# Kernel tuning notes

Hardware: AMD Instinct MI355X
Metric: run time of the kernel (lower is better)

## Reference

```python
import jax, jax.numpy as jnp
import numpy as np

M, U, H, C, EMB, HID = 4096, 8, 8, 64, 64, 128
N = M * U            # 32768 nodes
E = 131072           # edges
D = H * C            # 512 = heads * hidden_channels
NUM_LAYERS = 4
IN0 = 6              # 2 coords + mask + speed + cost + arrival
SCALE = np.float32(1.0 / np.sqrt(C))

def _lin(x, W, b):
    return x @ W + b

def _transformer_conv(x, src, dst, Wq, bq, Wk, bk, Wv, bv, Ws, bs):
    # PyG TransformerConv: x_j = x[src], x_i = x[dst]; softmax over edges per dst
    n = x.shape[0]
    q = _lin(x, Wq, bq).reshape(n, H, C)
    k = _lin(x, Wk, bk).reshape(n, H, C)
    v = _lin(x, Wv, bv).reshape(n, H, C)
    alpha = jnp.einsum('ehc,ehc->eh', q[dst], k[src]) * SCALE   # [E,H]
    amax = jax.ops.segment_max(alpha, dst, num_segments=n)       # [N,H]
    ex = jnp.exp(alpha - amax[dst])
    denom = jax.ops.segment_sum(ex, dst, num_segments=n)         # [N,H]
    agg = jax.ops.segment_sum(ex[:, :, None] * v[src], dst, num_segments=n)  # [N,H,C]
    out = agg / (denom[:, :, None] + 1e-16)
    return out.reshape(n, D) + _lin(x, Ws, bs)                   # concat heads + root skip

def _forward(mission_coords, uavs_info, speeds, cost_matrix, arrival_times,
             Wq0, bq0, Wk0, bk0, Wv0, bv0, Ws0, bs0,
             Wq, bq, Wk, bk, Wv, bv, Ws, bs,
             fc_W, fc_b, aW1, ab1, aW2, ab2, cW1, cb1, cW2, cb2,
             edge_index, batch, action_mask):
    mc = jnp.broadcast_to(mission_coords[:, None, :], (M, U, 2))
    mk = jnp.broadcast_to(action_mask[:, None, None].astype(jnp.float32), (M, U, 1))
    sp = jnp.broadcast_to(speeds[None, :, None], (M, U, 1))
    cm = cost_matrix.T[:, :, None]
    at = arrival_times.T[:, :, None]
    x = jnp.concatenate([mc, mk, sp, cm, at], axis=-1).reshape(N, IN0)
    src, dst = edge_index[0], edge_index[1]
    x = jax.nn.relu(_transformer_conv(x, src, dst, Wq0, bq0, Wk0, bk0, Wv0, bv0, Ws0, bs0))
    for l in range(NUM_LAYERS - 1):
        x = jax.nn.relu(_transformer_conv(x, src, dst, Wq[l], bq[l], Wk[l], bk[l], Wv[l], bv[l], Ws[l], bs[l]))
    new_batch = jnp.repeat(batch, U)                             # [N]
    sums = jax.ops.segment_sum(x, new_batch, num_segments=1)
    cnts = jax.ops.segment_sum(jnp.ones((N,), x.dtype), new_batch, num_segments=1)
    pooled = sums / cnts[:, None]                                # [1, D]
    emb = _lin(pooled, fc_W, fc_b)                               # [1, EMB]
    emb_exp = jnp.tile(emb, (U, 1))                              # [U, EMB]
    combined = jnp.concatenate([uavs_info, emb_exp, speeds[:, None]], axis=-1)  # [U, EMB+3]
    action_probs = jax.nn.softmax(_lin(jax.nn.relu(_lin(combined, aW1, ab1)), aW2, ab2), axis=-1)
    state_values = _lin(jax.nn.relu(_lin(combined, cW1, cb1)), cW2, cb2)
    return action_probs, state_values

def setup_inputs() -> dict:
    key = jax.random.key(0)
    ks = jax.random.split(key, 40)
    def nrm(i, shape, s=0.05):
        return jax.random.normal(ks[i], shape, jnp.float32) * s
    z = lambda *s: jnp.zeros(s, jnp.float32)
    L = NUM_LAYERS - 1
    inp = dict(
        mission_coords=jax.random.uniform(ks[0], (M, 2), jnp.float32),
        uavs_info=nrm(1, (U, 2), 1.0),
        speeds=jax.random.uniform(ks[2], (U,), jnp.float32) + 0.5,
        cost_matrix=jax.random.uniform(ks[3], (U, M), jnp.float32),
        arrival_times=jax.random.uniform(ks[4], (U, M), jnp.float32),
        edge_index=jax.random.randint(ks[5], (2, E), 0, N),
        batch=jnp.zeros((M,), jnp.int32),
        action_mask=jax.random.randint(ks[6], (M,), 0, 2),
        Wq0=nrm(7, (IN0, D)), bq0=z(D), Wk0=nrm(8, (IN0, D)), bk0=z(D),
        Wv0=nrm(9, (IN0, D)), bv0=z(D), Ws0=nrm(10, (IN0, D)), bs0=z(D),
        Wq=nrm(11, (L, D, D)), bq=z(L, D), Wk=nrm(12, (L, D, D)), bk=z(L, D),
        Wv=nrm(13, (L, D, D)), bv=z(L, D), Ws=nrm(14, (L, D, D)), bs=z(L, D),
        fc_W=nrm(15, (D, EMB)), fc_b=z(EMB),
        aW1=nrm(16, (EMB + 3, HID)), ab1=z(HID), aW2=nrm(17, (HID, M)), ab2=z(M),
        cW1=nrm(18, (EMB + 3, HID)), cb1=z(HID), cW2=nrm(19, (HID, 1)), cb2=z(1),
    )
    return inp

def reference(mission_coords, edge_index, batch, uavs_info, action_mask, speeds,
              cost_matrix, arrival_times,
              Wq0, bq0, Wk0, bk0, Wv0, bv0, Ws0, bs0,
              Wq, bq, Wk, bk, Wv, bv, Ws, bs,
              fc_W, fc_b, aW1, ab1, aW2, ab2, cW1, cb1, cW2, cb2):
    return _forward(mission_coords, uavs_info, speeds, cost_matrix, arrival_times,
                    Wq0, bq0, Wk0, bk0, Wv0, bv0, Ws0, bs0,
                    Wq, bq, Wk, bk, Wv, bv, Ws, bs,
                    fc_W, fc_b, aW1, ab1, aW2, ab2, cW1, cb1, cW2, cb2,
                    edge_index, batch, action_mask)
```

## Files before the change

### kernel.cpp

```cpp
#include <hip/hip_runtime.h>
#include <stdint.h>

typedef unsigned char u8;
typedef unsigned short u16;
typedef unsigned long long u64;
typedef __attribute__((ext_vector_type(8))) unsigned short u16x8;
typedef __attribute__((ext_vector_type(8))) __bf16 bf16x8;
typedef __attribute__((ext_vector_type(4))) float f32x4;
typedef __attribute__((ext_vector_type(2))) float f32x2;

#define NNODES 32768
#define NEDGES 131072
#define DDIM 512
#define QK4 2048
#define MM 4096
#define UU 8


__device__ __forceinline__ u16 f2bf(float f) {
    unsigned u = __builtin_bit_cast(unsigned, f);
    u += 0x7FFFu + ((u >> 16) & 1u);
    return (u16)(u >> 16);
}
__device__ __forceinline__ float bf2f(u16 h) {
    return __builtin_bit_cast(float, (unsigned)h << 16);
}
__device__ __forceinline__ void enc8(const float* f, int* lo, int* hi) {
    int a = __builtin_amdgcn_cvt_pk_fp8_f32(f[0], f[1], 0, false);
    a = __builtin_amdgcn_cvt_pk_fp8_f32(f[2], f[3], a, true);
    int b = __builtin_amdgcn_cvt_pk_fp8_f32(f[4], f[5], 0, false);
    b = __builtin_amdgcn_cvt_pk_fp8_f32(f[6], f[7], b, true);
    *lo = a;
    *hi = b;
}
__device__ __forceinline__ void dec8(int lo, int hi, float* f) {
    f32x2 a = __builtin_amdgcn_cvt_pk_f32_fp8(lo, false);
    f32x2 b = __builtin_amdgcn_cvt_pk_f32_fp8(lo, true);
    f32x2 c = __builtin_amdgcn_cvt_pk_f32_fp8(hi, false);
    f32x2 d = __builtin_amdgcn_cvt_pk_f32_fp8(hi, true);
    f[0] = a[0]; f[1] = a[1]; f[2] = b[0]; f[3] = b[1];
    f[4] = c[0]; f[5] = c[1]; f[6] = d[0]; f[7] = d[1];
}

__device__ __forceinline__ void load_lds16(const void* g, void* l) {
    __builtin_amdgcn_global_load_lds((__attribute__((address_space(1))) unsigned int*)(void*)g,
                                     (__attribute__((address_space(3))) unsigned int*)l, 16, 0, 0);
}

__global__ void k_prep(const float* __restrict__ mc, const int* __restrict__ mask,
                       const float* __restrict__ sp, const float* __restrict__ cm,
                       const float* __restrict__ at, float* __restrict__ x0,
                       const float* __restrict__ Wq0, const float* __restrict__ Wk0,
                       const float* __restrict__ Wv0, const float* __restrict__ Ws0,
                       float* __restrict__ W0cat,
                       const float* __restrict__ bq0, const float* __restrict__ bk0,
                       const float* __restrict__ bv0, const float* __restrict__ bs0,
                       const float* __restrict__ bq, const float* __restrict__ bk,
                       const float* __restrict__ bv, const float* __restrict__ bs,
                       float* __restrict__ b0cat, float* __restrict__ bcat,
                       int* __restrict__ deg, float* __restrict__ pooled) {
    int b = blockIdx.x;
    int t = threadIdx.x;
    if (b < 128) {
        int node = b * 256 + t;
        deg[node] = 0;
        int m = node >> 3, u = node & 7;
        float* o = x0 + (size_t)node * 6;
        o[0] = mc[m * 2];
        o[1] = mc[m * 2 + 1];
        o[2] = (float)mask[m];
        o[3] = sp[u];
        o[4] = cm[u * MM + m];
        o[5] = at[u * MM + m];
    } else if (b < 176) {
        int i = (b - 128) * 256 + t;
        int k = i / QK4, n = i % QK4;
        int ty = n >> 9, nn = n & 511;
        const float* p = (ty == 0) ? Wq0 : (ty == 1) ? Wk0 : (ty == 2) ? Wv0 : Ws0;
        W0cat[i] = p[k * DDIM + nn];
    } else if (b < 208) {
        int i = (b - 176) * 256 + t;
        int n = i & (QK4 - 1);
        int l = i >> 11;
        int ty = n >> 9, nn = n & 511;
        if (l == 0) {
            const float* p = (ty == 0) ? bq0 : (ty == 1) ? bk0 : (ty == 2) ? bv0 : bs0;
            b0cat[n] = p[nn];
        } else {
            const float* p = (ty == 0) ? bq : (ty == 1) ? bk : (ty == 2) ? bv : bs;
            bcat[(size_t)(l - 1) * QK4 + n] = p[(l - 1) * DDIM + nn];
        }
    } else {
        pooled[(b - 208) * 256 + t] = 0.f;
    }
}

__global__ void k_wt(const float* __restrict__ Wq, const float* __restrict__ Wk,
                     const float* __restrict__ Wv, const float* __restrict__ Ws,
                     u16* __restrict__ Wt) {
    __shared__ float tile[32][33];
    int q = blockIdx.z;
    int l = q >> 2, t = q & 3;
    const float* src = ((t == 0) ? Wq : (t == 1) ? Wk : (t == 2) ? Wv : Ws) + (size_t)l * DDIM * DDIM;
    int k0 = blockIdx.x * 32, n0 = blockIdx.y * 32;
    int tx = threadIdx.x, ty = threadIdx.y;
#pragma unroll
    for (int r = 0; r < 4; r++) tile[ty + 8 * r][tx] = src[(size_t)(k0 + ty + 8 * r) * DDIM + n0 + tx];
    __syncthreads();
    u16* dst = Wt + (size_t)l * QK4 * DDIM + (size_t)t * DDIM * DDIM;
#pragma unroll
    for (int r = 0; r < 4; r++) {
        int n = n0 + ty + 8 * r;
        dst[(size_t)n * DDIM + k0 + tx] = f2bf(tile[tx][ty + 8 * r]);
    }
}

__global__ void k_count(const int* __restrict__ dst, int* __restrict__ deg) {
    int e = blockIdx.x * 256 + threadIdx.x;
    if (e < NEDGES) atomicAdd(&deg[dst[e]], 1);
}

__global__ __launch_bounds__(1024) void k_scan(const int* __restrict__ deg, int* __restrict__ offs,
                                               int* __restrict__ cursor) {
    __shared__ int sums[1024];
    int t = threadIdx.x;
    int base = t * 32;
    int local[32];
    int s = 0;
#pragma unroll
    for (int i = 0; i < 32; i++) { local[i] = s; s += deg[base + i]; }
    sums[t] = s;
    __syncthreads();
    for (int d = 1; d < 1024; d <<= 1) {
        int v = (t >= d) ? sums[t - d] : 0;
        __syncthreads();
        sums[t] += v;
        __syncthreads();
    }
    int excl = (t == 0) ? 0 : sums[t - 1];
#pragma unroll
    for (int i = 0; i < 32; i++) {
        int o = excl + local[i];
        offs[base + i] = o;
        cursor[base + i] = o;
    }
    if (t == 1023) offs[NNODES] = sums[1023];
}

__global__ void k_scatter(const int* __restrict__ src, const int* __restrict__ dst,
                          int* __restrict__ cursor, int* __restrict__ ssrc) {
    int e = blockIdx.x * 256 + threadIdx.x;
    if (e < NEDGES) {
        int pos = atomicAdd(&cursor[dst[e]], 1);
        ssrc[pos] = src[e];
    }
}

__global__ __launch_bounds__(256) void k_gemm0(const float* __restrict__ x0, const float* __restrict__ W0cat,
                                               const float* __restrict__ b0cat, u8* __restrict__ Q8,
                                               u8* __restrict__ KV8, u16* __restrict__ S16) {
    int node = blockIdx.x;
    int t = threadIdx.x;
    float xv[6];
#pragma unroll
    for (int k = 0; k < 6; k++) xv[k] = x0[(size_t)node * 6 + k];
    int n0 = t * 8;
    float f[8];
#pragma unroll
    for (int j = 0; j < 8; j++) {
        int n = n0 + j;
        float s = b0cat[n];
#pragma unroll
        for (int k = 0; k < 6; k++) s += xv[k] * W0cat[k * QK4 + n];
        f[j] = s;
    }
    if (n0 < 512) {
        int lo, hi;
        enc8(f, &lo, &hi);
        *(int2*)(Q8 + (size_t)node * 512 + n0) = make_int2(lo, hi);
    } else if (n0 < 1536) {
        int lo, hi;
        enc8(f, &lo, &hi);
        int kvcol = (n0 < 1024) ? (n0 - 512) : (n0 - 1024);
        int ofs = (n0 < 1024) ? 0 : 8;
        *(int2*)(KV8 + (size_t)node * 1024 + (size_t)(kvcol >> 3) * 16 + ofs) = make_int2(lo, hi);
    } else {
        u16x8 o;
#pragma unroll
        for (int j = 0; j < 8; j++) o[j] = f2bf(f[j]);
        *(u16x8*)(S16 + (size_t)node * 512 + (n0 - 1536)) = o;
    }
}

__global__ __launch_bounds__(256, 4) void k_gemm(const u16* __restrict__ X, const u16* __restrict__ Wt,
                                                 const float* __restrict__ bcat, u8* __restrict__ Q8,
                                                 u8* __restrict__ KV8, u16* __restrict__ S16) {
    __shared__ __align__(16) u16 smem[2 * 128 * 64];
    u16* As = smem;
    u16* Bs = smem + 128 * 64;
    const int tid = threadIdx.x;
    const int lane = tid & 63;
    const int w = tid >> 6;
    const int wm = w & 1, wn = w >> 1;
    const int bid = blockIdx.x;
    const int xcd = bid & 7;
    const int s = bid >> 3;
    const size_t arow0 = (size_t)(xcd * 32 + (s >> 4)) * 128;
    const size_t brow0 = (size_t)(s & 15) * 128;
    const int bt = (int)(brow0 >> 7);

    f32x4 acc[4][4];
#pragma unroll
    for (int i = 0; i < 4; i++)
#pragma unroll
        for (int j = 0; j < 4; j++) acc[i][j] = (f32x4){0.f, 0.f, 0.f, 0.f};

    const int la = lane & 7;
    const int quad = lane >> 4;
    const int lm = lane & 15;

    for (int kt = 0; kt < 8; ++kt) {
        const int k0 = kt * 64;
#pragma unroll
        for (int t = 0; t < 4; ++t) {
            int idx = (w * 4 + t) * 64 + lane;
            int m = idx >> 3;
            int c = la ^ (m & 7);
            const u16* ga = X + (arow0 + m) * DDIM + (k0 + c * 8);
            const u16* gb = Wt + (brow0 + m) * DDIM + (k0 + c * 8);
            load_lds16(ga, &As[(size_t)((w * 4 + t) * 64) * 8]);
            load_lds16(gb, &Bs[(size_t)((w * 4 + t) * 64) * 8]);
        }
        __syncthreads();
#pragma unroll
        for (int kk = 0; kk < 2; ++kk) {
            bf16x8 af[4], bfg[4];
            int c = kk * 4 + quad;
#pragma unroll
            for (int i = 0; i < 4; ++i) {
                int m = wm * 64 + i * 16 + lm;
                int slot = m * 8 + (c ^ (m & 7));
                af[i] = *(const bf16x8*)&As[(size_t)slot * 8];
            }
#pragma unroll
            for (int j = 0; j < 4; ++j) {
                int n = wn * 64 + j * 16 + lm;
                int slot = n * 8 + (c ^ (n & 7));
                bfg[j] = *(const bf16x8*)&Bs[(size_t)slot * 8];
            }
#pragma unroll
            for (int i = 0; i < 4; ++i)
#pragma unroll
                for (int j = 0; j < 4; ++j)
                    acc[i][j] = __builtin_amdgcn_mfma_f32_16x16x32_bf16(af[i], bfg[j], acc[i][j], 0, 0, 0);
        }
        __syncthreads();
    }

    float biasv[4];
#pragma unroll
    for (int j = 0; j < 4; ++j) biasv[j] = bcat[brow0 + wn * 64 + j * 16 + lm];

    u16* stg = smem;
    const int chunk = lane & 7;
    const int rrow = lane >> 3;
    const int colbase = (int)brow0 + wn * 64 + chunk * 8;
#pragma unroll
    for (int p = 0; p < 2; ++p) {
        __syncthreads();
#pragma unroll
        for (int ii = 0; ii < 2; ++ii) {
            int i = p * 2 + ii;
#pragma unroll
            for (int j = 0; j < 4; ++j) {
#pragma unroll
                for (int r = 0; r < 4; ++r) {
                    int lr = ii * 16 + quad * 4 + r;
                    int lc = j * 16 + lm;
                    stg[(size_t)(w * 32 + lr) * 72 + lc] = f2bf(acc[i][j][r] + biasv[j]);
                }
            }
        }
        __syncthreads();
#pragma unroll
        for (int it = 0; it < 4; ++it) {
            int row = it * 8 + rrow;
            u16x8 v = *(const u16x8*)&stg[(size_t)(w * 32 + row) * 72 + chunk * 8];
            size_t grow = arow0 + wm * 64 + p * 32 + row;
            if (bt < 4) {
                float f[8];
#pragma unroll
                for (int j = 0; j < 8; j++) f[j] = bf2f(v[j]);
                int lo, hi;
                enc8(f, &lo, &hi);
                *(int2*)(Q8 + grow * 512 + colbase) = make_int2(lo, hi);
            } else if (bt < 12) {
                float f[8];
#pragma unroll
                for (int j = 0; j < 8; j++) f[j] = bf2f(v[j]);
                int lo, hi;
                enc8(f, &lo, &hi);
                int kvcol = (bt < 8) ? (colbase - 512) : (colbase - 1024);
                int ofs = (bt < 8) ? 0 : 8;
                *(int2*)(KV8 + grow * 1024 + (size_t)(kvcol >> 3) * 16 + ofs) = make_int2(lo, hi);
            } else {
                *(u16x8*)(S16 + grow * 512 + (colbase - 1536)) = v;
            }
        }
    }
}

__global__ __launch_bounds__(256) void k_attn(const u8* __restrict__ Q8, const u8* __restrict__ KV8,
                                              const u16* __restrict__ S16, const int* __restrict__ offs,
                                              const int* __restrict__ ssrc, u16* __restrict__ Xout) {
    const int lane = threadIdx.x & 63;
    const int node = blockIdx.x * 4 + (threadIdx.x >> 6);
    const u64 q8 = *(const u64*)(Q8 + (size_t)node * 512 + (size_t)lane * 8);
    float qf[8];
    dec8((int)(q8 & 0xFFFFFFFFull), (int)(q8 >> 32), qf);
    float m = -INFINITY, l = 0.f;
    float acc[8];
#pragma unroll
    for (int j = 0; j < 8; j++) acc[j] = 0.f;
    const int e0 = offs[node], e1 = offs[node + 1];
    int4 kvn;
    if (e0 < e1) kvn = *(const int4*)(KV8 + (size_t)ssrc[e0] * 1024 + (size_t)lane * 16);
    for (int e = e0; e < e1; ++e) {
        int4 kv = kvn;
        if (e + 1 < e1) kvn = *(const int4*)(KV8 + (size_t)ssrc[e + 1] * 1024 + (size_t)lane * 16);
        f32x2 k01 = __builtin_amdgcn_cvt_pk_f32_fp8(kv.x, false);
        f32x2 k23 = __builtin_amdgcn_cvt_pk_f32_fp8(kv.x, true);
        f32x2 k45 = __builtin_amdgcn_cvt_pk_f32_fp8(kv.y, false);
        f32x2 k67 = __builtin_amdgcn_cvt_pk_f32_fp8(kv.y, true);
        float d = qf[0] * k01[0] + qf[1] * k01[1] + qf[2] * k23[0] + qf[3] * k23[1] +
                  qf[4] * k45[0] + qf[5] * k45[1] + qf[6] * k67[0] + qf[7] * k67[1];
        d += __shfl_xor(d, 1, 64);
        d += __shfl_xor(d, 2, 64);
        d += __shfl_xor(d, 4, 64);
        float a = d * 0.125f;
        float nm = fmaxf(m, a);
        float corr = __expf(m - nm);
        float p = __expf(a - nm);
        l = l * corr + p;
        f32x2 v01 = __builtin_amdgcn_cvt_pk_f32_fp8(kv.z, false);
        f32x2 v23 = __builtin_amdgcn_cvt_pk_f32_fp8(kv.z, true);
        f32x2 v45 = __builtin_amdgcn_cvt_pk_f32_fp8(kv.w, false);
        f32x2 v67 = __builtin_amdgcn_cvt_pk_f32_fp8(kv.w, true);
        acc[0] = acc[0] * corr + p * v01[0];
        acc[1] = acc[1] * corr + p * v01[1];
        acc[2] = acc[2] * corr + p * v23[0];
        acc[3] = acc[3] * corr + p * v23[1];
        acc[4] = acc[4] * corr + p * v45[0];
        acc[5] = acc[5] * corr + p * v45[1];
        acc[6] = acc[6] * corr + p * v67[0];
        acc[7] = acc[7] * corr + p * v67[1];
        m = nm;
    }
    float inv = 1.0f / (l + 1e-16f);
    const u16x8 sv = *(const u16x8*)(S16 + (size_t)node * 512 + (size_t)lane * 8);
    u16x8 o;
#pragma unroll
    for (int j = 0; j < 8; j++) {
        float r = acc[j] * inv + bf2f(sv[j]);
        o[j] = f2bf(fmaxf(r, 0.f));
    }
    *(u16x8*)(Xout + (size_t)node * DDIM + (size_t)lane * 8) = o;
}

__global__ __launch_bounds__(256) void k_pool(const u16* __restrict__ X, float* __restrict__ pooled) {
    __shared__ float red[4][64][8];
    int t = threadIdx.x;
    int chunk = t & 63;
    int rofs = t >> 6;
    float s[8];
#pragma unroll
    for (int j = 0; j < 8; j++) s[j] = 0.f;
    int nd0 = blockIdx.x * 256;
    for (int nd = nd0 + rofs; nd < nd0 + 256; nd += 4) {
        u16x8 v = *(const u16x8*)&X[(size_t)nd * DDIM + chunk * 8];
#pragma unroll
        for (int j = 0; j < 8; j++) s[j] += bf2f(v[j]);
    }
#pragma unroll
    for (int j = 0; j < 8; j++) red[rofs][chunk][j] = s[j];
    __syncthreads();
    if (t < 64) {
#pragma unroll
        for (int j = 0; j < 8; j++) {
            float o = red[0][t][j] + red[1][t][j] + red[2][t][j] + red[3][t][j];
            atomicAdd(&pooled[t * 8 + j], o);
        }
    }
}

__global__ __launch_bounds__(1024) void k_heads(const float* __restrict__ pooled, const float* __restrict__ fcW,
                                                const float* __restrict__ fcb, const float* __restrict__ ui,
                                                const float* __restrict__ sp, const float* __restrict__ aW1,
                                                const float* __restrict__ ab1, const float* __restrict__ cW1,
                                                const float* __restrict__ cb1, const float* __restrict__ cW2,
                                                const float* __restrict__ cb2, float* __restrict__ hidden_a,
                                                float* __restrict__ out) {
    __shared__ float spool[512];
    __shared__ float semb[64];
    __shared__ float shc[8][128];
    int t = threadIdx.x;
    if (t < 512) spool[t] = pooled[t] * (1.0f / 32768.0f);
    __syncthreads();
    if (t < 64) {
        float s = fcb[t];
        for (int k = 0; k < 512; k++) s += spool[k] * fcW[k * 64 + t];
        semb[t] = s;
    }
    __syncthreads();
    int u = t >> 7, j = t & 127;
    float u0 = ui[u * 2], u1 = ui[u * 2 + 1], uspd = sp[u];
    float ha = ab1[j] + u0 * aW1[j] + u1 * aW1[128 + j] + uspd * aW1[66 * 128 + j];
    float hc = cb1[j] + u0 * cW1[j] + u1 * cW1[128 + j] + uspd * cW1[66 * 128 + j];
    for (int k = 0; k < 64; k++) {
        float e = semb[k];
        ha += e * aW1[(2 + k) * 128 + j];
        hc += e * cW1[(2 + k) * 128 + j];
    }
    ha = fmaxf(ha, 0.f);
    hc = fmaxf(hc, 0.f);
    hidden_a[u * 128 + j] = ha;
    shc[u][j] = hc;
    __syncthreads();
    if (t < 8) {
        float s = cb2[0];
        for (int k = 0; k < 128; k++) s += shc[t][k] * cW2[k];
        out[NNODES + t] = s;
    }
}

__global__ __launch_bounds__(1024) void k_actor(const float* __restrict__ hidden_a, const float* __restrict__ aW2,
                                                const float* __restrict__ ab2, float* __restrict__ out) {
    __shared__ float h[128];
    __shared__ float red[1024];
    int u = blockIdx.x, t = threadIdx.x;
    if (t < 128) h[t] = hidden_a[u * 128 + t];
    __syncthreads();
    float lg[4];
#pragma unroll
    for (int p = 0; p < 4; p++) {
        int mcol = t + p * 1024;
        float s = ab2[mcol];
        for (int k = 0; k < 128; k++) s += h[k] * aW2[(size_t)k * MM + mcol];
        lg[p] = s;
    }
    float mx = fmaxf(fmaxf(lg[0], lg[1]), fmaxf(lg[2], lg[3]));
    red[t] = mx;
    __syncthreads();
    for (int s2 = 512; s2 > 0; s2 >>= 1) {
        if (t < s2) red[t] = fmaxf(red[t], red[t + s2]);
        __syncthreads();
    }
    mx = red[0];
    __syncthreads();
    float e[4], sum = 0.f;
#pragma unroll
    for (int p = 0; p < 4; p++) {
        e[p] = __expf(lg[p] - mx);
        sum += e[p];
    }
    red[t] = sum;
    __syncthreads();
    for (int s2 = 512; s2 > 0; s2 >>= 1) {
        if (t < s2) red[t] += red[t + s2];
        __syncthreads();
    }
    float inv = 1.0f / red[0];
#pragma unroll
    for (int p = 0; p < 4; p++) out[(size_t)u * MM + t + p * 1024] = e[p] * inv;
}

extern "C" void kernel_launch(void* const* d_in, const int* in_sizes, int n_in,
                              void* d_out, int out_size, void* d_ws, size_t ws_size,
                              hipStream_t stream) {
    const float* mc   = (const float*)d_in[0];
    const float* ui   = (const float*)d_in[1];
    const float* sp   = (const float*)d_in[2];
    const float* cm   = (const float*)d_in[3];
    const float* at   = (const float*)d_in[4];
    const int*   eidx = (const int*)d_in[5];
    const int*   mask = (const int*)d_in[7];
    const float* Wq0 = (const float*)d_in[8];
    const float* bq0 = (const float*)d_in[9];
    const float* Wk0 = (const float*)d_in[10];
    const float* bk0 = (const float*)d_in[11];
    const float* Wv0 = (const float*)d_in[12];
    const float* bv0 = (const float*)d_in[13];
    const float* Ws0 = (const float*)d_in[14];
    const float* bs0 = (const float*)d_in[15];
    const float* Wq = (const float*)d_in[16];
    const float* bq = (const float*)d_in[17];
    const float* Wk = (const float*)d_in[18];
    const float* bk = (const float*)d_in[19];
    const float* Wv = (const float*)d_in[20];
    const float* bv = (const float*)d_in[21];
    const float* Ws = (const float*)d_in[22];
    const float* bs = (const float*)d_in[23];
    const float* fcW = (const float*)d_in[24];
    const float* fcb = (const float*)d_in[25];
    const float* aW1 = (const float*)d_in[26];
    const float* ab1 = (const float*)d_in[27];
    const float* aW2 = (const float*)d_in[28];
    const float* ab2 = (const float*)d_in[29];
    const float* cW1 = (const float*)d_in[30];
    const float* cb1 = (const float*)d_in[31];
    const float* cW2 = (const float*)d_in[32];
    const float* cb2 = (const float*)d_in[33];
    float* out = (float*)d_out;

    const int* esrc = eidx;
    const int* edst = eidx + NEDGES;

    char* ws = (char*)d_ws;
    size_t off = 0;
    auto alloc = [&](size_t bytes) -> void* {
        void* p = ws + off;
        off += (bytes + 255) & ~(size_t)255;
        return p;
    };
    u8*    Q8    = (u8*)alloc((size_t)NNODES * 512);
    u8*    KV8   = (u8*)alloc((size_t)NNODES * 1024);
    u16*   S16   = (u16*)alloc((size_t)NNODES * 512 * 2);
    u16*   X     = (u16*)alloc((size_t)NNODES * DDIM * 2);
    u16*   Wt    = (u16*)alloc((size_t)3 * QK4 * DDIM * 2);
    float* W0cat = (float*)alloc((size_t)6 * QK4 * 4);
    float* b0cat = (float*)alloc((size_t)QK4 * 4);
    float* bcat  = (float*)alloc((size_t)3 * QK4 * 4);
    float* x0    = (float*)alloc((size_t)NNODES * 6 * 4);
    int*   deg   = (int*)alloc((size_t)NNODES * 4);
    int*   offs  = (int*)alloc((size_t)(NNODES + 1) * 4);
    int*   cursor= (int*)alloc((size_t)NNODES * 4);
    int*   ssrc  = (int*)alloc((size_t)NEDGES * 4);
    float* pooled= (float*)alloc((size_t)512 * 4);
    float* hidden_a = (float*)alloc((size_t)UU * 128 * 4);
    (void)ws_size; (void)in_sizes; (void)n_in; (void)out_size;

    k_prep<<<210, 256, 0, stream>>>(mc, mask, sp, cm, at, x0, Wq0, Wk0, Wv0, Ws0, W0cat,
                                    bq0, bk0, bv0, bs0, bq, bk, bv, bs, b0cat, bcat, deg, pooled);
    {
        dim3 g(16, 16, 12), b(32, 8);
        k_wt<<<g, b, 0, stream>>>(Wq, Wk, Wv, Ws, Wt);
    }
    k_count<<<NEDGES / 256, 256, 0, stream>>>(edst, deg);
    k_scan<<<1, 1024, 0, stream>>>(deg, offs, cursor);
    k_scatter<<<NEDGES / 256, 256, 0, stream>>>(esrc, edst, cursor, ssrc);

    k_gemm0<<<NNODES, 256, 0, stream>>>(x0, W0cat, b0cat, Q8, KV8, S16);
    k_attn<<<NNODES / 4, 256, 0, stream>>>(Q8, KV8, S16, offs, ssrc, X);

    for (int l = 0; l < 3; ++l) {
        k_gemm<<<4096, 256, 0, stream>>>(X, Wt + (size_t)l * QK4 * DDIM, bcat + (size_t)l * QK4, Q8, KV8, S16);
        k_attn<<<NNODES / 4, 256, 0, stream>>>(Q8, KV8, S16, offs, ssrc, X);
    }

    k_pool<<<128, 256, 0, stream>>>(X, pooled);
    k_heads<<<1, 1024, 0, stream>>>(pooled, fcW, fcb, ui, sp, aW1, ab1, cW1, cb1, cW2, cb2, hidden_a, out);
    k_actor<<<UU, 1024, 0, stream>>>(hidden_a, aW2, ab2, out);
}
```

Before: 631.0 us.

## Collapse first TransformerConv layer into low-rank bilinear attention on 6-dim inputs

Layer 0 inputs have only 6 features, so the per-head score q_i·k_j is rewritten as a 6x6 bilinear form plus linear and constant terms, precomputed once in a tiny kernel. The attention loop then aggregates the raw 6-dim source features weighted by softmax, and projects them through Wv0 afterwards, which removes the layer-0 gemm and its Q/KV/S writes and reads. Separately, the main attention loop now loads up to four neighbour KV rows at once instead of prefetching one ahead. This adds more per-edge scalar arithmetic and larger register pressure in k_attn0, and skips the fp8 quantisation the old layer-0 path applied to Q, K and V.

```diff
diff --git a/kernel.cpp b/kernel.cpp
--- a/kernel.cpp
+++ b/kernel.cpp
@@ -50,14 +50,9 @@
 __global__ void k_prep(const float* __restrict__ mc, const int* __restrict__ mask,
                        const float* __restrict__ sp, const float* __restrict__ cm,
                        const float* __restrict__ at, float* __restrict__ x0,
-                       const float* __restrict__ Wq0, const float* __restrict__ Wk0,
-                       const float* __restrict__ Wv0, const float* __restrict__ Ws0,
-                       float* __restrict__ W0cat,
-                       const float* __restrict__ bq0, const float* __restrict__ bk0,
-                       const float* __restrict__ bv0, const float* __restrict__ bs0,
                        const float* __restrict__ bq, const float* __restrict__ bk,
                        const float* __restrict__ bv, const float* __restrict__ bs,
-                       float* __restrict__ b0cat, float* __restrict__ bcat,
+                       float* __restrict__ bcat,
                        int* __restrict__ deg, float* __restrict__ pooled) {
     int b = blockIdx.x;
     int t = threadIdx.x;
@@ -72,27 +67,39 @@
         o[3] = sp[u];
         o[4] = cm[u * MM + m];
         o[5] = at[u * MM + m];
-    } else if (b < 176) {
+    } else if (b < 152) {
         int i = (b - 128) * 256 + t;
-        int k = i / QK4, n = i % QK4;
-        int ty = n >> 9, nn = n & 511;
-        const float* p = (ty == 0) ? Wq0 : (ty == 1) ? Wk0 : (ty == 2) ? Wv0 : Ws0;
-        W0cat[i] = p[k * DDIM + nn];
-    } else if (b < 208) {
-        int i = (b - 176) * 256 + t;
         int n = i & (QK4 - 1);
         int l = i >> 11;
         int ty = n >> 9, nn = n & 511;
-        if (l == 0) {
-            const float* p = (ty == 0) ? bq0 : (ty == 1) ? bk0 : (ty == 2) ? bv0 : bs0;
-            b0cat[n] = p[nn];
-        } else {
-            const float* p = (ty == 0) ? bq : (ty == 1) ? bk : (ty == 2) ? bv : bs;
-            bcat[(size_t)(l - 1) * QK4 + n] = p[(l - 1) * DDIM + nn];
-        }
+        const float* p = (ty == 0) ? bq : (ty == 1) ? bk : (ty == 2) ? bv : bs;
+        bcat[(size_t)l * QK4 + n] = p[l * DDIM + nn];
     } else {
-        pooled[(b - 208) * 256 + t] = 0.f;
-    }
+        pooled[(b - 152) * 256 + t] = 0.f;
+    }
+}
+
+__global__ void k_c0(const float* __restrict__ Wq0, const float* __restrict__ bq0,
+                     const float* __restrict__ Wk0, const float* __restrict__ bk0,
+                     float* __restrict__ C0) {
+    int i = threadIdx.x;
+    if (i >= 392) return;
+    int h = i / 49, r = i % 49;
+    int d0 = h * 64;
+    float s = 0.f;
+    if (r < 36) {
+        int a = r / 6, b = r % 6;
+        for (int d = 0; d < 64; d++) s += Wq0[a * DDIM + d0 + d] * Wk0[b * DDIM + d0 + d];
+    } else if (r < 42) {
+        int a = r - 36;
+        for (int d = 0; d < 64; d++) s += Wq0[a * DDIM + d0 + d] * bk0[d0 + d];
+    } else if (r < 48) {
+        int b = r - 42;
+        for (int d = 0; d < 64; d++) s += Wk0[b * DDIM + d0 + d] * bq0[d0 + d];
+    } else {
+        for (int d = 0; d < 64; d++) s += bq0[d0 + d] * bk0[d0 + d];
+    }
+    C0[i] = s;
 }
 
 __global__ void k_wt(const float* __restrict__ Wq, const float* __restrict__ Wk,
@@ -156,39 +163,82 @@
     }
 }
 
-__global__ __launch_bounds__(256) void k_gemm0(const float* __restrict__ x0, const float* __restrict__ W0cat,
-                                               const float* __restrict__ b0cat, u8* __restrict__ Q8,
-                                               u8* __restrict__ KV8, u16* __restrict__ S16) {
-    int node = blockIdx.x;
-    int t = threadIdx.x;
-    float xv[6];
-#pragma unroll
-    for (int k = 0; k < 6; k++) xv[k] = x0[(size_t)node * 6 + k];
-    int n0 = t * 8;
-    float f[8];
-#pragma unroll
-    for (int j = 0; j < 8; j++) {
-        int n = n0 + j;
-        float s = b0cat[n];
-#pragma unroll
-        for (int k = 0; k < 6; k++) s += xv[k] * W0cat[k * QK4 + n];
-        f[j] = s;
-    }
-    if (n0 < 512) {
-        int lo, hi;
-        enc8(f, &lo, &hi);
-        *(int2*)(Q8 + (size_t)node * 512 + n0) = make_int2(lo, hi);
-    } else if (n0 < 1536) {
-        int lo, hi;
-        enc8(f, &lo, &hi);
-        int kvcol = (n0 < 1024) ? (n0 - 512) : (n0 - 1024);
-        int ofs = (n0 < 1024) ? 0 : 8;
-        *(int2*)(KV8 + (size_t)node * 1024 + (size_t)(kvcol >> 3) * 16 + ofs) = make_int2(lo, hi);
-    } else {
-        u16x8 o;
-#pragma unroll
-        for (int j = 0; j < 8; j++) o[j] = f2bf(f[j]);
-        *(u16x8*)(S16 + (size_t)node * 512 + (n0 - 1536)) = o;
+__global__ __launch_bounds__(256) void k_attn0(const float* __restrict__ x0, const float* __restrict__ C0,
+                                               const float* __restrict__ Wv0, const float* __restrict__ bv0,
+                                               const float* __restrict__ Ws0, const float* __restrict__ bs0,
+                                               const int* __restrict__ offs, const int* __restrict__ ssrc,
+                                               u16* __restrict__ Xout) {
+    const int lane = threadIdx.x & 63;
+    const int wv = threadIdx.x >> 6;
+    const int h = lane & 7;
+    float wV[8][6], wS[8][6], bV[8], bS[8];
+#pragma unroll
+    for (int j = 0; j < 8; ++j) {
+        int c = lane + 64 * j;
+        bV[j] = bv0[c];
+        bS[j] = bs0[c];
+#pragma unroll
+        for (int a = 0; a < 6; ++a) {
+            wV[j][a] = Wv0[a * DDIM + c];
+            wS[j][a] = Ws0[a * DDIM + c];
+        }
+    }
+    float Ah[36], uh[6], wh[6], ch;
+#pragma unroll
+    for (int r = 0; r < 36; ++r) Ah[r] = C0[h * 49 + r];
+#pragma unroll
+    for (int a = 0; a < 6; ++a) uh[a] = C0[h * 49 + 36 + a];
+#pragma unroll
+    for (int a = 0; a < 6; ++a) wh[a] = C0[h * 49 + 42 + a];
+    ch = C0[h * 49 + 48];
+
+    int node0 = (blockIdx.x * 4 + wv) * 8;
+    for (int nn = 0; nn < 8; ++nn) {
+        int node = node0 + nn;
+        float xi[6];
+#pragma unroll
+        for (int a = 0; a < 6; ++a) xi[a] = x0[(size_t)node * 6 + a];
+        float m = -INFINITY, l = 0.f;
+        float xh[6];
+#pragma unroll
+        for (int a = 0; a < 6; ++a) xh[a] = 0.f;
+        const int e0 = offs[node], e1 = offs[node + 1];
+        for (int e = e0; e < e1; ++e) {
+            int s = ssrc[e];
+            float xj[6];
+#pragma unroll
+            for (int a = 0; a < 6; ++a) xj[a] = x0[(size_t)s * 6 + a];
+            float alpha = ch;
+#pragma unroll
+            for (int a = 0; a < 6; ++a) {
+                float t = uh[a];
+#pragma unroll
+                for (int b = 0; b < 6; ++b) t += Ah[a * 6 + b] * xj[b];
+                alpha += xi[a] * t;
+            }
+#pragma unroll
+            for (int b = 0; b < 6; ++b) alpha += wh[b] * xj[b];
+            alpha *= 0.125f;
+            float nm = fmaxf(m, alpha);
+            float corr = __expf(m - nm);
+            float p = __expf(alpha - nm);
+            l = l * corr + p;
+#pragma unroll
+            for (int a = 0; a < 6; ++a) xh[a] = xh[a] * corr + p * xj[a];
+            m = nm;
+        }
+#pragma unroll
+        for (int j = 0; j < 8; ++j) {
+            float lb = __shfl(l, j, 64);
+            float num = lb * bV[j];
+#pragma unroll
+            for (int a = 0; a < 6; ++a) num += __shfl(xh[a], j, 64) * wV[j][a];
+            float skip = bS[j];
+#pragma unroll
+            for (int a = 0; a < 6; ++a) skip += xi[a] * wS[j][a];
+            float r = num / (lb + 1e-16f) + skip;
+            Xout[(size_t)node * DDIM + lane + 64 * j] = f2bf(fmaxf(r, 0.f));
+        }
     }
 }
 
@@ -323,38 +373,51 @@
 #pragma unroll
     for (int j = 0; j < 8; j++) acc[j] = 0.f;
     const int e0 = offs[node], e1 = offs[node + 1];
-    int4 kvn;
-    if (e0 < e1) kvn = *(const int4*)(KV8 + (size_t)ssrc[e0] * 1024 + (size_t)lane * 16);
-    for (int e = e0; e < e1; ++e) {
-        int4 kv = kvn;
-        if (e + 1 < e1) kvn = *(const int4*)(KV8 + (size_t)ssrc[e + 1] * 1024 + (size_t)lane * 16);
-        f32x2 k01 = __builtin_amdgcn_cvt_pk_f32_fp8(kv.x, false);
-        f32x2 k23 = __builtin_amdgcn_cvt_pk_f32_fp8(kv.x, true);
-        f32x2 k45 = __builtin_amdgcn_cvt_pk_f32_fp8(kv.y, false);
-        f32x2 k67 = __builtin_amdgcn_cvt_pk_f32_fp8(kv.y, true);
-        float d = qf[0] * k01[0] + qf[1] * k01[1] + qf[2] * k23[0] + qf[3] * k23[1] +
-                  qf[4] * k45[0] + qf[5] * k45[1] + qf[6] * k67[0] + qf[7] * k67[1];
-        d += __shfl_xor(d, 1, 64);
-        d += __shfl_xor(d, 2, 64);
-        d += __shfl_xor(d, 4, 64);
-        float a = d * 0.125f;
-        float nm = fmaxf(m, a);
-        float corr = __expf(m - nm);
-        float p = __expf(a - nm);
-        l = l * corr + p;
-        f32x2 v01 = __builtin_amdgcn_cvt_pk_f32_fp8(kv.z, false);
-        f32x2 v23 = __builtin_amdgcn_cvt_pk_f32_fp8(kv.z, true);
-        f32x2 v45 = __builtin_amdgcn_cvt_pk_f32_fp8(kv.w, false);
-        f32x2 v67 = __builtin_amdgcn_cvt_pk_f32_fp8(kv.w, true);
-        acc[0] = acc[0] * corr + p * v01[0];
-        acc[1] = acc[1] * corr + p * v01[1];
-        acc[2] = acc[2] * corr + p * v23[0];
-        acc[3] = acc[3] * corr + p * v23[1];
-        acc[4] = acc[4] * corr + p * v45[0];
-        acc[5] = acc[5] * corr + p * v45[1];
-        acc[6] = acc[6] * corr + p * v67[0];
-        acc[7] = acc[7] * corr + p * v67[1];
-        m = nm;
+    int e = e0;
+    while (e < e1) {
+        int nb = e1 - e;
+        if (nb > 4) nb = 4;
+        int4 kvb[4];
+#pragma unroll
+        for (int i = 0; i < 4; ++i) {
+            if (i < nb) {
+                int s = ssrc[e + i];
+                kvb[i] = *(const int4*)(KV8 + (size_t)s * 1024 + (size_t)lane * 16);
+            }
+        }
+#pragma unroll
+        for (int i = 0; i < 4; ++i) {
+            if (i >= nb) break;
+            int4 kv = kvb[i];
+            f32x2 k01 = __builtin_amdgcn_cvt_pk_f32_fp8(kv.x, false);
+            f32x2 k23 = __builtin_amdgcn_cvt_pk_f32_fp8(kv.x, true);
+            f32x2 k45 = __builtin_amdgcn_cvt_pk_f32_fp8(kv.y, false);
+            f32x2 k67 = __builtin_amdgcn_cvt_pk_f32_fp8(kv.y, true);
+            float d = qf[0] * k01[0] + qf[1] * k01[1] + qf[2] * k23[0] + qf[3] * k23[1] +
+                      qf[4] * k45[0] + qf[5] * k45[1] + qf[6] * k67[0] + qf[7] * k67[1];
+            d += __shfl_xor(d, 1, 64);
+            d += __shfl_xor(d, 2, 64);
+            d += __shfl_xor(d, 4, 64);
+            float a = d * 0.125f;
+            float nm = fmaxf(m, a);
+            float corr = __expf(m - nm);
+            float p = __expf(a - nm);
+            l = l * corr + p;
+            f32x2 v01 = __builtin_amdgcn_cvt_pk_f32_fp8(kv.z, false);
+            f32x2 v23 = __builtin_amdgcn_cvt_pk_f32_fp8(kv.z, true);
+            f32x2 v45 = __builtin_amdgcn_cvt_pk_f32_fp8(kv.w, false);
+            f32x2 v67 = __builtin_amdgcn_cvt_pk_f32_fp8(kv.w, true);
+            acc[0] = acc[0] * corr + p * v01[0];
+            acc[1] = acc[1] * corr + p * v01[1];
+            acc[2] = acc[2] * corr + p * v23[0];
+            acc[3] = acc[3] * corr + p * v23[1];
+            acc[4] = acc[4] * corr + p * v45[0];
+            acc[5] = acc[5] * corr + p * v45[1];
+            acc[6] = acc[6] * corr + p * v67[0];
+            acc[7] = acc[7] * corr + p * v67[1];
+            m = nm;
+        }
+        e += nb;
     }
     float inv = 1.0f / (l + 1e-16f);
     const u16x8 sv = *(const u16x8*)(S16 + (size_t)node * 512 + (size_t)lane * 8);
@@ -527,9 +590,8 @@
     u16*   S16   = (u16*)alloc((size_t)NNODES * 512 * 2);
     u16*   X     = (u16*)alloc((size_t)NNODES * DDIM * 2);
     u16*   Wt    = (u16*)alloc((size_t)3 * QK4 * DDIM * 2);
-    float* W0cat = (float*)alloc((size_t)6 * QK4 * 4);
-    float* b0cat = (float*)alloc((size_t)QK4 * 4);
     float* bcat  = (float*)alloc((size_t)3 * QK4 * 4);
+    float* C0    = (float*)alloc((size_t)392 * 4);
     float* x0    = (float*)alloc((size_t)NNODES * 6 * 4);
     int*   deg   = (int*)alloc((size_t)NNODES * 4);
     int*   offs  = (int*)alloc((size_t)(NNODES + 1) * 4);
@@ -539,8 +601,8 @@
     float* hidden_a = (float*)alloc((size_t)UU * 128 * 4);
     (void)ws_size; (void)in_sizes; (void)n_in; (void)out_size;
 
-    k_prep<<<210, 256, 0, stream>>>(mc, mask, sp, cm, at, x0, Wq0, Wk0, Wv0, Ws0, W0cat,
-                                    bq0, bk0, bv0, bs0, bq, bk, bv, bs, b0cat, bcat, deg, pooled);
+    k_prep<<<154, 256, 0, stream>>>(mc, mask, sp, cm, at, x0, bq, bk, bv, bs, bcat, deg, pooled);
+    k_c0<<<1, 512, 0, stream>>>(Wq0, bq0, Wk0, bk0, C0);
     {
         dim3 g(16, 16, 12), b(32, 8);
         k_wt<<<g, b, 0, stream>>>(Wq, Wk, Wv, Ws, Wt);
@@ -549,8 +611,7 @@
     k_scan<<<1, 1024, 0, stream>>>(deg, offs, cursor);
     k_scatter<<<NEDGES / 256, 256, 0, stream>>>(esrc, edst, cursor, ssrc);
 
-    k_gemm0<<<NNODES, 256, 0, stream>>>(x0, W0cat, b0cat, Q8, KV8, S16);
-    k_attn<<<NNODES / 4, 256, 0, stream>>>(Q8, KV8, S16, offs, ssrc, X);
+    k_attn0<<<1024, 256, 0, stream>>>(x0, C0, Wv0, bv0, Ws0, bs0, offs, ssrc, X);
 
     for (int l = 0; l < 3; ++l) {
         k_gemm<<<4096, 256, 0, stream>>>(X, Wt + (size_t)l * QK4 * DDIM, bcat + (size_t)l * QK4, Q8, KV8, S16);
```

After: 622.7 us. Within noise of the previous version (-1.3%).
